# Kernel tuning notes

Measured on AMD Instinct MI355X. Metric: run time of the kernel, lower is better.

## Reference

```python
import jax, jax.numpy as jnp
import numpy as np

SEQ, BS, DIM = 2048, 2, 256
G, NQ = 2, 8           # n_keys groups, n_queries total
SUB = NQ // G          # queries per group
EPS = 1e-5


def _ln(x, gamma, beta):
    m = jnp.mean(x, axis=-1, keepdims=True)
    v = jnp.mean(jnp.square(x - m), axis=-1, keepdims=True)
    return (x - m) * jax.lax.rsqrt(v + EPS) * gamma + beta


def setup_inputs() -> dict:
    key = jax.random.key(0)
    ks = jax.random.split(key, 16)
    s = 0.02
    return {
        "x":   jax.random.normal(ks[0], (SEQ, BS, DIM), jnp.float32),
        # block layernorms
        "g0": jnp.ones((DIM,), jnp.float32), "b0": jnp.zeros((DIM,), jnp.float32),
        "g1": jnp.ones((DIM,), jnp.float32), "b1": jnp.zeros((DIM,), jnp.float32),
        # attention q/k layernorm (norm_kvs=True)
        "gn": jnp.ones((DIM,), jnp.float32), "bn": jnp.zeros((DIM,), jnp.float32),
        # attention projections (torch Linear: weight [out,in])
        "wk": jax.random.normal(ks[1], (DIM * G, DIM), jnp.float32) * s,
        "bk": jnp.zeros((DIM * G,), jnp.float32),
        "wv": jax.random.normal(ks[2], (DIM * G, DIM), jnp.float32) * s,
        "bv": jnp.zeros((DIM * G,), jnp.float32),
        "wq": jax.random.normal(ks[3], (DIM * NQ, DIM), jnp.float32) * s,
        "bq": jnp.zeros((DIM * NQ,), jnp.float32),
        "wo": jax.random.normal(ks[4], (DIM, DIM * NQ), jnp.float32) * s,
        "bo": jnp.zeros((DIM,), jnp.float32),
        # FFN: BayesLora(dim,2dim) -> relu -> BayesLora(2dim,dim), eval == plain linear
        "w1": jax.random.normal(ks[5], (2 * DIM, DIM), jnp.float32) * s,
        "bf1": jnp.zeros((2 * DIM,), jnp.float32),
        "w2": jax.random.normal(ks[6], (DIM, 2 * DIM), jnp.float32) * s,
        "bf2": jnp.zeros((DIM,), jnp.float32),
    }


def reference(x, g0, b0, g1, b1, gn, bn, wk, bk, wv, bv, wq, bq, wo, bo, w1, bf1, w2, bf2):
    seq, bs, dim = x.shape
    # --- attention (pre-norm) ---
    h = _ln(x, g0, b0)                                        # s b d
    K = (h @ wk.T + bk).reshape(seq, bs, G, dim)              # s b g i
    V = (h @ wv.T + bv).reshape(seq, bs, G, dim)              # s b g i
    Q = (h @ wq.T + bq).reshape(seq, bs, G, SUB, dim)         # s b g u i
    K = _ln(K, gn, bn)
    Q = _ln(Q, gn, bn)
    scores = jnp.einsum('sbgui,tbgi->bgust', Q, K) / jnp.sqrt(jnp.float32(dim))
    neg = jnp.finfo(scores.dtype).min
    causal = jnp.tril(jnp.ones((seq, seq), bool))             # s1 >= s2 allowed
    scores = jnp.where(causal, scores, neg)
    probs = jax.nn.softmax(scores, axis=-1)                   # b g u s t
    out = jnp.einsum('bgust,tbgi->sbgui', probs, V)
    out = out.reshape(seq, bs, G * SUB * dim)                 # s b (g u i)
    x = x + (out @ wo.T + bo)
    # --- FFN (pre-norm) ---
    h2 = _ln(x, g1, b1)
    f = jax.nn.relu(h2 @ w1.T + bf1) @ w2.T + bf2
    return x + f
```

## Files before the change

kernel.cpp:

```cpp
#include <hip/hip_runtime.h>
#include <hip/hip_bf16.h>

#define SEQ  2048
#define BSZ  2
#define DIM  256
#define NG   2
#define NQH  8
#define SUBQ 4
#define ROWS (SEQ*BSZ)
#define NQKV 3072
#define QROW 6144

typedef unsigned int uint32;
typedef unsigned short ushort;
typedef __attribute__((ext_vector_type(8))) short short8;
typedef __attribute__((ext_vector_type(4))) float f32x4;

__device__ __forceinline__ float bflo(uint32 u){
  union { uint32 i; float f; } c; c.i = u << 16; return c.f;
}
__device__ __forceinline__ float bfhi(uint32 u){
  union { uint32 i; float f; } c; c.i = u & 0xffff0000u; return c.f;
}
__device__ __forceinline__ uint32 pack2(float a, float b){
  __hip_bfloat16 ha = __float2bfloat16(a);
  __hip_bfloat16 hb = __float2bfloat16(b);
  unsigned short ua, ub;
  __builtin_memcpy(&ua, &ha, 2);
  __builtin_memcpy(&ub, &hb, 2);
  return (uint32)ua | ((uint32)ub << 16);
}
__device__ __forceinline__ ushort bf16bits(float v){
  __hip_bfloat16 h = __float2bfloat16(v);
  ushort u; __builtin_memcpy(&u, &h, 2); return u;
}

__device__ __forceinline__ void dma16(const void* g, void* l) {
  __builtin_amdgcn_global_load_lds(
      (const __attribute__((address_space(1))) uint32*)g,
      (__attribute__((address_space(3))) uint32*)l, 16, 0, 0);
}

__device__ __forceinline__ size_t op2_addr(size_t o2) {
  return (o2 >> 11) * QROW + (o2 & 1023) + ((o2 >> 10) & 1) * 3072;
}

__global__ __launch_bounds__(256) void misc0(
    const float* __restrict__ wk, const float* __restrict__ wv,
    const float* __restrict__ wq, const float* __restrict__ wo,
    const float* __restrict__ w1, const float* __restrict__ w2,
    const float* __restrict__ bk, const float* __restrict__ bv,
    const float* __restrict__ bq,
    __hip_bfloat16* __restrict__ out, float* __restrict__ bc,
    const float* __restrict__ x, const float* __restrict__ g0,
    const float* __restrict__ b0, __hip_bfloat16* __restrict__ Hf)
{
  if (blockIdx.x < 771) {
    int u = blockIdx.x * 256 + threadIdx.x;
    if (u < 196608) {
      int lane = u & 63, col = lane & 15, quad = lane >> 4;
      const float* srcrow;
      if (u < 98304) {
        int n16 = u >> 9, kc = (u >> 6) & 7;
        int n = n16 * 16 + col;
        const float* m = (n < 512) ? (wk + (size_t)n * 256)
                       : (n < 1024) ? (wv + (size_t)(n - 512) * 256)
                                    : (wq + (size_t)(n - 1024) * 256);
        srcrow = m + kc * 32 + quad * 8;
      } else if (u < 163840) {
        int local = u - 98304;
        int n16 = local >> 12, kc = (local >> 6) & 63;
        srcrow = wo + (size_t)(n16 * 16 + col) * 2048 + kc * 32 + quad * 8;
      } else if (u < 180224) {
        int local = u - 163840;
        int n16 = local >> 9, kc = (local >> 6) & 7;
        srcrow = w1 + (size_t)(n16 * 16 + col) * 256 + kc * 32 + quad * 8;
      } else {
        int local = u - 180224;
        int n16 = local >> 10, kc = (local >> 6) & 15;
        srcrow = w2 + (size_t)(n16 * 16 + col) * 512 + kc * 32 + quad * 8;
      }
      float4 a = *(const float4*)srcrow;
      float4 b = *(const float4*)(srcrow + 4);
      uint4 st;
      st.x = pack2(a.x, a.y); st.y = pack2(a.z, a.w);
      st.z = pack2(b.x, b.y); st.w = pack2(b.z, b.w);
      *(uint4*)((ushort*)out + (size_t)u * 8) = st;
    } else {
      int bu = u - 196608;
      const float* src; int loc;
      if      (bu < 128) { src = bk; loc = bu; }
      else if (bu < 256) { src = bv; loc = bu - 128; }
      else               { src = bq; loc = bu - 256; }
      *(float4*)(bc + 4 * (size_t)bu) = *(const float4*)(src + 4 * (size_t)loc);
    }
  } else {
    int wave = threadIdx.x >> 6, lane = threadIdx.x & 63;
    int row = (blockIdx.x - 771) * 4 + wave;
    size_t base = (size_t)row * DIM + lane * 4;
    float4 v = *(const float4*)(x + base);
    float s  = v.x + v.y + v.z + v.w;
    float s2 = v.x*v.x + v.y*v.y + v.z*v.z + v.w*v.w;
    #pragma unroll
    for (int o = 1; o < 64; o <<= 1) {
      s  += __shfl_xor(s, o);
      s2 += __shfl_xor(s2, o);
    }
    float m = s * (1.0f / DIM);
    float rb = rsqrtf(s2 * (1.0f / DIM) - m * m + 1e-5f);
    float4 gm = *(const float4*)(g0 + lane * 4);
    float4 bt = *(const float4*)(b0 + lane * 4);
    uint2 st;
    st.x = pack2((v.x - m) * rb * gm.x + bt.x, (v.y - m) * rb * gm.y + bt.y);
    st.y = pack2((v.z - m) * rb * gm.z + bt.z, (v.w - m) * rb * gm.w + bt.w);
    int kc = lane >> 3, quad = (lane >> 1) & 3, jj = 4 * (lane & 1);
    int cid = (row >> 4) * 8 + kc;
    *(uint2*)((ushort*)Hf + (size_t)cid * 512 + (quad * 16 + (row & 15)) * 8 + jj) = st;
  }
}

__global__ __launch_bounds__(256) void ln_swz(
    __hip_bfloat16* __restrict__ QKV,
    const float* __restrict__ gamma, const float* __restrict__ beta,
    __hip_bfloat16* __restrict__ Kf, __hip_bfloat16* __restrict__ Vf)
{
  int j = blockIdx.x;
  if (j < 10240) {
    int wave = threadIdx.x >> 6, lane = threadIdx.x & 63;
    int idx = j * 4 + wave;
    size_t base;
    if (idx < 8192) base = (size_t)(idx >> 1) * NQKV + (idx & 1) * DIM;
    else {
      int qi = idx - 8192;
      base = (size_t)(qi >> 3) * NQKV + 2 * NG * DIM + (qi & 7) * DIM;
    }
    __hip_bfloat16* p = QKV + base + lane * 4;
    uint2 u = *(const uint2*)p;
    float v0 = bflo(u.x), v1 = bfhi(u.x), v2 = bflo(u.y), v3 = bfhi(u.y);
    float s  = v0 + v1 + v2 + v3;
    float s2 = v0*v0 + v1*v1 + v2*v2 + v3*v3;
    #pragma unroll
    for (int o = 1; o < 64; o <<= 1) {
      s  += __shfl_xor(s, o);
      s2 += __shfl_xor(s2, o);
    }
    float m = s * (1.0f / DIM);
    float rb = rsqrtf(s2 * (1.0f / DIM) - m * m + 1e-5f);
    float4 gm = *(const float4*)(gamma + lane * 4);
    float4 bt = *(const float4*)(beta + lane * 4);
    uint2 st;
    st.x = pack2((v0 - m) * rb * gm.x + bt.x, (v1 - m) * rb * gm.y + bt.y);
    st.y = pack2((v2 - m) * rb * gm.z + bt.z, (v3 - m) * rb * gm.w + bt.w);
    if (idx < 8192) {
      int r = idx >> 1, gg = idx & 1;
      int t = r >> 1, b = r & 1;
      int bg = b * NG + gg;
      int kt = t >> 5, tr = t & 31, tc = tr >> 4, col = tr & 15;
      int ks = lane >> 3, quad = (lane >> 1) & 3, jj = 4 * (lane & 1);
      int cid = (bg * 64 + kt) * 16 + tc * 8 + ks;
      *(uint2*)((ushort*)Kf + (size_t)cid * 512 + (quad * 16 + col) * 8 + jj) = st;
    } else {
      *(uint2*)p = st;
    }
  } else {
    __shared__ ushort T[64][72];
    int vb = j - 10240;
    int t0 = (vb & 31) * 64, d0 = ((vb >> 5) & 3) * 64, bg = vb >> 7;
    int b = bg >> 1, g = bg & 1;
    int tid = threadIdx.x;
    int tr = tid >> 2, c4 = (tid & 3) * 16;
    const ushort* src = (const ushort*)QKV + ((size_t)(t0 + tr) * BSZ + b) * NQKV
                      + NG * DIM + g * DIM + d0 + c4;
    uint4 a0 = *(const uint4*)src;
    uint4 a1 = *(const uint4*)(src + 8);
    *(uint4*)&T[tr][c4]     = a0;
    *(uint4*)&T[tr][c4 + 8] = a1;
    __syncthreads();
    #pragma unroll
    for (int k2 = 0; k2 < 2; ++k2) {
      int u = tid * 2 + k2;
      int tt = u >> 8, di = (u >> 6) & 3, qd = (u >> 4) & 3, cl = u & 15;
      ushort tmp[8];
      #pragma unroll
      for (int e = 0; e < 8; ++e) tmp[e] = T[tt * 32 + qd * 8 + e][di * 16 + cl];
      int kt = (t0 >> 5) + tt;
      int dc = (d0 >> 4) + di;
      *(uint4*)((ushort*)Vf + (((size_t)(bg * 64 + kt) * 16 + dc) << 9) + (qd * 16 + cl) * 8)
          = *(uint4*)tmp;
    }
  }
}

template<int GN, int RELU, int OUTMODE, int AFRAG>
__global__ __launch_bounds__(256) void gemm_mfma(
    const __hip_bfloat16* __restrict__ A,
    const __hip_bfloat16* __restrict__ W,
    const float* __restrict__ bias,
    const float* __restrict__ resid,
    void* __restrict__ outp,
    int M, int N, int K)
{
  constexpr int WCH = GN / 16;
  constexpr int MC  = (GN == 128) ? 4 : 2;
  __shared__ __align__(16) ushort AS[2][4096];
  __shared__ __align__(16) ushort WS[2][WCH * 512];

  const int tid = threadIdx.x;
  const int wave = tid >> 6, lane = tid & 63;
  const int col = lane & 15, quad = lane >> 4;
  const int wm = (GN == 128) ? (wave >> 1) : wave;
  const int wn = (GN == 128) ? (wave & 1) : 0;
  const int bn0 = blockIdx.x * GN;
  const int bm0 = blockIdx.y * 128;
  const bool SPLIT = (OUTMODE == 2 || OUTMODE == 4);
  const int Keff  = SPLIT ? (K / gridDim.z) : K;
  const int kbase = SPLIT ? blockIdx.z * Keff : 0;
  const int kiters = Keff >> 5;

  f32x4 acc[MC][4];
  #pragma unroll
  for (int mc = 0; mc < MC; ++mc)
    #pragma unroll
    for (int nc = 0; nc < 4; ++nc)
      acc[mc][nc] = (f32x4){0.f, 0.f, 0.f, 0.f};

  auto stage = [&](int it, int bufi) {
    int k0 = kbase + it * 32;
    #pragma unroll
    for (int c = 0; c < 2; ++c) {
      int ch = wave * 2 + c;
      if (AFRAG)
        dma16((const ushort*)A + ((((size_t)(bm0 >> 4) + ch) * (K >> 5) + (k0 >> 5)) << 9) + lane * 8,
              &AS[bufi][ch * 512]);
      else
        dma16((const ushort*)A + (size_t)(bm0 + ch * 16 + col) * K + k0 + quad * 8,
              &AS[bufi][ch * 512]);
    }
    #pragma unroll
    for (int c = 0; c < WCH / 4; ++c) {
      int ch = wave * (WCH / 4) + c;
      dma16((const ushort*)W + (((size_t)((bn0 >> 4) + ch) * (K >> 5) + (k0 >> 5)) << 9) + lane * 8,
            &WS[bufi][ch * 512]);
    }
  };

  stage(0, 0);
  for (int it = 0; it < kiters; ++it) {
    int cur = it & 1;
    __syncthreads();
    if (it + 1 < kiters) stage(it + 1, 1 - cur);
    short8 af[MC], bf_[4];
    #pragma unroll
    for (int mc = 0; mc < MC; ++mc)
      af[mc] = *(const short8*)&AS[cur][(wm * MC + mc) * 512 + lane * 8];
    #pragma unroll
    for (int nc = 0; nc < 4; ++nc)
      bf_[nc] = *(const short8*)&WS[cur][(wn * 4 + nc) * 512 + lane * 8];
    #pragma unroll
    for (int mc = 0; mc < MC; ++mc)
      #pragma unroll
      for (int nc = 0; nc < 4; ++nc)
        acc[mc][nc] = __builtin_amdgcn_mfma_f32_16x16x32_bf16(af[mc], bf_[nc], acc[mc][nc], 0, 0, 0);
  }

  #pragma unroll
  for (int nc = 0; nc < 4; ++nc) {
    int n = bn0 + wn * 64 + nc * 16 + col;
    float bv = 0.f;
    if (OUTMODE == 0 || OUTMODE == 1 || OUTMODE == 3) bv = bias[n];
    #pragma unroll
    for (int mc = 0; mc < MC; ++mc) {
      #pragma unroll
      for (int reg = 0; reg < 4; ++reg) {
        int m = bm0 + wm * (MC * 16) + mc * 16 + quad * 4 + reg;
        float v = acc[mc][nc][reg] + bv;
        if ((OUTMODE == 0 || OUTMODE == 1 || OUTMODE == 3) && resid)
          v += resid[(size_t)m * N + n];
        if (RELU) v = fmaxf(v, 0.f);
        if (OUTMODE == 0)
          ((__hip_bfloat16*)outp)[(size_t)m * N + n] = __float2bfloat16(v);
        else if (OUTMODE == 1)
          ((float*)outp)[(size_t)m * N + n] = v;
        else if (OUTMODE == 2)
          ((float*)outp)[(size_t)blockIdx.z * M * N + (size_t)m * N + n] = v;
        else if (OUTMODE == 3) {
          int cid = (m >> 4) * (N >> 5) + (n >> 5);
          int kl = n & 31;
          ((ushort*)outp)[(size_t)cid * 512 + ((kl >> 3) * 16 + (m & 15)) * 8 + (kl & 7)] = bf16bits(v);
        } else {
          ((ushort*)outp)[(size_t)blockIdx.z * M * N + (size_t)m * N + n] = bf16bits(v);
        }
      }
    }
  }
}

__global__ __launch_bounds__(256) void combine2(
    const ushort* __restrict__ P, const float* __restrict__ bias,
    const float* __restrict__ resid, float* __restrict__ out, int MN)
{
  int i4 = (blockIdx.x * 256 + threadIdx.x) * 4;
  uint2 a = *(const uint2*)(P + i4);
  uint2 b = *(const uint2*)(P + MN + i4);
  float4 r = *(const float4*)(resid + i4);
  float4 bb = *(const float4*)(bias + (i4 & (DIM - 1)));
  float4 o;
  o.x = bflo(a.x) + bflo(b.x) + r.x + bb.x;
  o.y = bfhi(a.x) + bfhi(b.x) + r.y + bb.y;
  o.z = bflo(a.y) + bflo(b.y) + r.z + bb.z;
  o.w = bfhi(a.y) + bfhi(b.y) + r.w + bb.w;
  *(float4*)(out + i4) = o;
}

__global__ __launch_bounds__(256) void combine_ln4(
    const ushort* __restrict__ P, const float* __restrict__ bias,
    const float* __restrict__ resid, float* __restrict__ X2,
    const float* __restrict__ gamma, const float* __restrict__ beta,
    __hip_bfloat16* __restrict__ H2f)
{
  const int MN = ROWS * DIM;
  int wave = threadIdx.x >> 6, lane = threadIdx.x & 63;
  int row = blockIdx.x * 4 + wave;
  size_t i = (size_t)row * DIM + lane * 4;
  uint2 a = *(const uint2*)(P + i);
  uint2 b = *(const uint2*)(P + MN + i);
  uint2 c = *(const uint2*)(P + 2 * (size_t)MN + i);
  uint2 d = *(const uint2*)(P + 3 * (size_t)MN + i);
  float4 r = *(const float4*)(resid + i);
  float4 bb = *(const float4*)(bias + lane * 4);
  float4 v;
  v.x = bflo(a.x) + bflo(b.x) + bflo(c.x) + bflo(d.x) + r.x + bb.x;
  v.y = bfhi(a.x) + bfhi(b.x) + bfhi(c.x) + bfhi(d.x) + r.y + bb.y;
  v.z = bflo(a.y) + bflo(b.y) + bflo(c.y) + bflo(d.y) + r.z + bb.z;
  v.w = bfhi(a.y) + bfhi(b.y) + bfhi(c.y) + bfhi(d.y) + r.w + bb.w;
  *(float4*)(X2 + i) = v;
  float s  = v.x + v.y + v.z + v.w;
  float s2 = v.x*v.x + v.y*v.y + v.z*v.z + v.w*v.w;
  #pragma unroll
  for (int o = 1; o < 64; o <<= 1) {
    s  += __shfl_xor(s, o);
    s2 += __shfl_xor(s2, o);
  }
  float m = s * (1.0f / DIM);
  float rb = rsqrtf(s2 * (1.0f / DIM) - m * m + 1e-5f);
  float4 gm = *(const float4*)(gamma + lane * 4);
  float4 bt = *(const float4*)(beta + lane * 4);
  uint2 st;
  st.x = pack2((v.x - m) * rb * gm.x + bt.x, (v.y - m) * rb * gm.y + bt.y);
  st.y = pack2((v.z - m) * rb * gm.z + bt.z, (v.w - m) * rb * gm.w + bt.w);
  int kc = lane >> 3, quad = (lane >> 1) & 3, jj = 4 * (lane & 1);
  int cid = (row >> 4) * 8 + kc;
  *(uint2*)((ushort*)H2f + (size_t)cid * 512 + (quad * 16 + (row & 15)) * 8 + jj) = st;
}

__constant__ int C_NIT[32] = {22,22,22,21,21,20,20,20,20,20,20,19,19,18,18,18,18,17,17,16,16,16,16,16,16,14,14,12,12,12, 8, 4};
__constant__ int C_QB [32] = {10,10,15,15,15, 4, 9, 9,14,14,14,13,13,13, 8, 8,12,12,12, 3, 7, 7,11,11,11, 6, 6, 2, 5, 5, 1, 0};
__constant__ int C_Z  [32] = { 0, 1, 0, 1, 2, 0, 0, 1, 0, 1, 2, 0, 1, 2, 0, 1, 0, 1, 2, 0, 0, 1, 0, 1, 2, 0, 1, 0, 0, 1, 0, 0};
__constant__ int C_K0 [32] = { 0,22, 0,22,43, 0, 0,20, 0,20,40, 0,19,38, 0,18, 0,18,35, 0, 0,16, 0,16,32, 0,14, 0, 0,12, 0, 0};
__constant__ int C_SP [32] = { 1, 1, 1, 1, 1, 0, 1, 1, 1, 1, 1, 1, 1, 1, 1, 1, 1, 1, 1, 0, 1, 1, 1, 1, 1, 1, 1, 0, 1, 1, 0, 0};

__global__ __launch_bounds__(256, 2) void attn_mfma(
    const __hip_bfloat16* QKV,
    const __hip_bfloat16* __restrict__ Kf,
    const __hip_bfloat16* __restrict__ Vf,
    __hip_bfloat16* __restrict__ Obf,
    __hip_bfloat16* __restrict__ Op1f,
    ushort* Op2q,
    float* __restrict__ Lp)
{
  __shared__ __align__(16) ushort KS[2][8192];
  __shared__ __align__(16) ushort VS[2][8192];

  const int tid  = threadIdx.x;
  const int wave = tid >> 6, lane = tid & 63;
  const int col  = lane & 15, quad = lane >> 4;

  const int bid = blockIdx.x;
  const int x8 = bid & 7, j = bid >> 3;
  const int a = j >> 1, odd = j & 1;
  int rank;
  if (a < 16) rank = odd ? (31 - a) : a;
  else        rank = odd ? (a - 16) : (31 - (a - 16));
  const int head = odd * 8 + x8;
  const int qb  = C_QB[rank];
  const int z   = C_Z[rank];
  const int nit = C_NIT[rank];
  const int k0  = C_K0[rank];
  const int split = C_SP[rank];

  const int b = head >> 3, hq = head & 7, g = hq >> 2;
  const int bg = b * NG + g;
  const int qw0 = qb * 128 + wave * 32;

  short8 qf[2][8];
  #pragma unroll
  for (int mc = 0; mc < 2; ++mc) {
    int s = qw0 + mc * 16 + col;
    const ushort* qp = (const ushort*)QKV + (size_t)s * QROW + b * NQKV
                     + 2 * NG * DIM + hq * DIM + quad * 8;
    #pragma unroll
    for (int ks = 0; ks < 8; ++ks)
      qf[mc][ks] = *(const short8*)(qp + ks * 32);
  }

  short8 onesf;
  #pragma unroll
  for (int i = 0; i < 8; ++i) onesf[i] = (short)0x3F80;

  f32x4 o[2][16];
  #pragma unroll
  for (int mc = 0; mc < 2; ++mc)
    #pragma unroll
    for (int dc = 0; dc < 16; ++dc)
      o[mc][dc] = (f32x4){0.f, 0.f, 0.f, 0.f};
  float l_s[2][4] = {{0.f}};

  auto stage = [&](int i, int bufi) {
    int kt = k0 + i;
    const ushort* kb = (const ushort*)Kf + (((size_t)bg * 64 + kt) << 13);
    const ushort* vb = (const ushort*)Vf + (((size_t)bg * 64 + kt) << 13);
    #pragma unroll
    for (int cc = 0; cc < 4; ++cc) {
      int nk = wave * 4 + cc;
      dma16(kb + (nk << 9) + lane * 8, &KS[bufi][nk * 512]);
      dma16(vb + (nk << 9) + lane * 8, &VS[bufi][nk * 512]);
    }
  };

  const int sig0 = col + 16 * ((quad & 1) * 2);
  const int sig1 = sig0 + 16;

  stage(0, 0);
  for (int i = 0; i < nit; ++i) {
    int cur = i & 1;
    __syncthreads();
    if (i + 1 < nit) stage(i + 1, 1 - cur);
    int kt = k0 + i;
    if (kt * 32 > qw0 + 31) continue;

    f32x4 sf[2][2];
    #pragma unroll
    for (int mc = 0; mc < 2; ++mc)
      #pragma unroll
      for (int tc = 0; tc < 2; ++tc)
        sf[mc][tc] = (f32x4){0.f, 0.f, 0.f, 0.f};
    __builtin_amdgcn_s_setprio(1);
    #pragma unroll
    for (int ks = 0; ks < 8; ++ks) {
      short8 kb0 = *(const short8*)&KS[cur][ks * 512 + lane * 8];
      short8 kb1 = *(const short8*)&KS[cur][(8 + ks) * 512 + lane * 8];
      sf[0][0] = __builtin_amdgcn_mfma_f32_16x16x32_bf16(kb0, qf[0][ks], sf[0][0], 0, 0, 0);
      sf[0][1] = __builtin_amdgcn_mfma_f32_16x16x32_bf16(kb1, qf[0][ks], sf[0][1], 0, 0, 0);
      sf[1][0] = __builtin_amdgcn_mfma_f32_16x16x32_bf16(kb0, qf[1][ks], sf[1][0], 0, 0, 0);
      sf[1][1] = __builtin_amdgcn_mfma_f32_16x16x32_bf16(kb1, qf[1][ks], sf[1][1], 0, 0, 0);
    }
    __builtin_amdgcn_s_setprio(0);

    const bool dm = (kt * 32 + 31) > qw0;
    uint32 PK[2][2][2];
    #pragma unroll
    for (int mc = 0; mc < 2; ++mc)
      #pragma unroll
      for (int tc = 0; tc < 2; ++tc) {
        float p[4];
        #pragma unroll
        for (int reg = 0; reg < 4; ++reg) {
          p[reg] = __expf(sf[mc][tc][reg] * 0.0625f);
          if (dm) {
            int tg = kt * 32 + tc * 16 + quad * 4 + reg;
            int sg = qw0 + mc * 16 + col;
            if (tg > sg) p[reg] = 0.f;
          }
        }
        PK[mc][tc][0] = pack2(p[0], p[1]);
        PK[mc][tc][1] = pack2(p[2], p[3]);
      }

    short8 pa[2];
    #pragma unroll
    for (int mc = 0; mc < 2; ++mc) {
      union { uint32 u[4]; short8 s8; } cvt;
      #pragma unroll
      for (int dw = 0; dw < 4; ++dw) {
        int src = (dw < 2) ? sig0 : sig1;
        uint32 a0 = (uint32)__shfl((int)PK[mc][0][dw & 1], src, 64);
        uint32 a1 = (uint32)__shfl((int)PK[mc][1][dw & 1], src, 64);
        cvt.u[dw] = (quad < 2) ? a0 : a1;
      }
      pa[mc] = cvt.s8;
    }

    __builtin_amdgcn_s_setprio(1);
    f32x4 zz = (f32x4){0.f, 0.f, 0.f, 0.f};
    f32x4 ps0 = __builtin_amdgcn_mfma_f32_16x16x32_bf16(pa[0], onesf, zz, 0, 0, 0);
    f32x4 ps1 = __builtin_amdgcn_mfma_f32_16x16x32_bf16(pa[1], onesf, zz, 0, 0, 0);
    #pragma unroll
    for (int r = 0; r < 4; ++r) { l_s[0][r] += ps0[r]; l_s[1][r] += ps1[r]; }

    #pragma unroll
    for (int dc = 0; dc < 16; ++dc) {
      short8 vb = *(const short8*)&VS[cur][dc * 512 + lane * 8];
      o[0][dc] = __builtin_amdgcn_mfma_f32_16x16x32_bf16(pa[0], vb, o[0][dc], 0, 0, 0);
      o[1][dc] = __builtin_amdgcn_mfma_f32_16x16x32_bf16(pa[1], vb, o[1][dc], 0, 0, 0);
    }
    __builtin_amdgcn_s_setprio(0);
  }

  const int colh = col >> 3, coll = col & 7;
  #pragma unroll
  for (int mc = 0; mc < 2; ++mc)
    #pragma unroll
    for (int reg = 0; reg < 4; ++reg) {
      int s = qw0 + mc * 16 + quad * 4 + reg;
      int m = s * BSZ + b;
      int m16 = m >> 4, ml = m & 15;
      if (!split) {
        float inv = 1.0f / l_s[mc][reg];
        #pragma unroll
        for (int dc = 0; dc < 16; ++dc) {
          int cid = m16 * 64 + hq * 8 + (dc >> 1);
          int qt = (dc & 1) * 2 + colh;
          Obf[(size_t)cid * 512 + (qt * 16 + ml) * 8 + coll] =
              __float2bfloat16(o[mc][dc][reg] * inv);
        }
      } else {
        #pragma unroll
        for (int dc = 0; dc < 16; ++dc) {
          int qt = (dc & 1) * 2 + colh;
          int el = (qt * 16 + ml) * 8 + coll;
          float v = o[mc][dc][reg];
          if (z == 0) {
            Obf[((size_t)(m16 * 64 + hq * 8 + (dc >> 1))) * 512 + el] = __float2bfloat16(v);
          } else if (z == 1) {
            Op1f[((size_t)((m16 - 80) * 64 + hq * 8 + (dc >> 1))) * 512 + el] = __float2bfloat16(v);
          } else {
            size_t o2 = ((size_t)((m16 - 176) * 64 + hq * 8 + (dc >> 1))) * 512 + el;
            Op2q[op2_addr(o2)] = bf16bits(v);
          }
        }
        if (col == 0) Lp[((size_t)z * 2048 + s) * 16 + head] = l_s[mc][reg];
      }
    }
}

__global__ __launch_bounds__(256) void attn_norm(
    __hip_bfloat16* __restrict__ Obf, const __hip_bfloat16* __restrict__ Op1f,
    const ushort* __restrict__ Op2q, const float* __restrict__ Lp)
{
  int i8 = blockIdx.x * 256 + threadIdx.x;
  int cidr = i8 >> 6;
  int lane = i8 & 63;
  int m16r = cidr >> 6, kc = cidr & 63;
  int m16 = m16r + 80;
  int m = m16 * 16 + (lane & 15);
  int k = kc * 32 + (lane >> 4) * 8;
  int s = m >> 1, b = m & 1, hq = k >> 8;
  int head = b * 8 + hq;
  float l = Lp[(size_t)s * 16 + head] + Lp[(size_t)(2048 + s) * 16 + head];
  ushort* a = (ushort*)Obf + (((size_t)m16 * 64 + kc) << 9) + lane * 8;
  const ushort* c = (const ushort*)Op1f + (((size_t)m16r * 64 + kc) << 9) + lane * 8;
  uint4 ua = *(const uint4*)a;
  uint4 uc = *(const uint4*)c;
  float v0 = bflo(ua.x) + bflo(uc.x), v1 = bfhi(ua.x) + bfhi(uc.x);
  float v2 = bflo(ua.y) + bflo(uc.y), v3 = bfhi(ua.y) + bfhi(uc.y);
  float v4 = bflo(ua.z) + bflo(uc.z), v5 = bfhi(ua.z) + bfhi(uc.z);
  float v6 = bflo(ua.w) + bflo(uc.w), v7 = bfhi(ua.w) + bfhi(uc.w);
  if (s >= 1408) {
    l += Lp[(size_t)(4096 + s) * 16 + head];
    size_t o2 = (((size_t)(m16 - 176) * 64 + kc) << 9) + lane * 8;
    uint4 ue = *(const uint4*)(Op2q + op2_addr(o2));
    v0 += bflo(ue.x); v1 += bfhi(ue.x);
    v2 += bflo(ue.y); v3 += bfhi(ue.y);
    v4 += bflo(ue.z); v5 += bfhi(ue.z);
    v6 += bflo(ue.w); v7 += bfhi(ue.w);
  }
  float inv = 1.0f / l;
  uint4 st;
  st.x = pack2(v0 * inv, v1 * inv);
  st.y = pack2(v2 * inv, v3 * inv);
  st.z = pack2(v4 * inv, v5 * inv);
  st.w = pack2(v6 * inv, v7 * inv);
  *(uint4*)a = st;
}

extern "C" void kernel_launch(void* const* d_in, const int* in_sizes, int n_in,
                              void* d_out, int out_size, void* d_ws, size_t ws_size,
                              hipStream_t stream)
{
  const float* x   = (const float*)d_in[0];
  const float* g0  = (const float*)d_in[1];
  const float* b0  = (const float*)d_in[2];
  const float* g1  = (const float*)d_in[3];
  const float* b1  = (const float*)d_in[4];
  const float* gn  = (const float*)d_in[5];
  const float* bn  = (const float*)d_in[6];
  const float* wk  = (const float*)d_in[7];
  const float* bk  = (const float*)d_in[8];
  const float* wv  = (const float*)d_in[9];
  const float* bv  = (const float*)d_in[10];
  const float* wq  = (const float*)d_in[11];
  const float* bq  = (const float*)d_in[12];
  const float* wo  = (const float*)d_in[13];
  const float* bo  = (const float*)d_in[14];
  const float* w1  = (const float*)d_in[15];
  const float* bf1 = (const float*)d_in[16];
  const float* w2  = (const float*)d_in[17];
  const float* bf2 = (const float*)d_in[18];

  char* ws = (char*)d_ws;
  const size_t MB = 1024 * 1024;
  __hip_bfloat16* QKV = (__hip_bfloat16*)(ws);
  __hip_bfloat16* Pwo = (__hip_bfloat16*)(ws);
  __hip_bfloat16* Pw2 = (__hip_bfloat16*)(ws + 8  * MB);
  float*          X2  = (float*)         (ws + 16 * MB);
  __hip_bfloat16* H2f = (__hip_bfloat16*)(ws + 20 * MB);
  __hip_bfloat16* F1f = (__hip_bfloat16*)(ws + 22 * MB);
  __hip_bfloat16* Hf  = (__hip_bfloat16*)(ws + 24 * MB);
  __hip_bfloat16* Kf  = (__hip_bfloat16*)(ws + 24 * MB);
  __hip_bfloat16* Vf  = (__hip_bfloat16*)(ws + 28 * MB);
  __hip_bfloat16* Obf = (__hip_bfloat16*)(ws + 32 * MB);
  __hip_bfloat16* Op1f= (__hip_bfloat16*)(ws + 48 * MB);
  float*          BC  = (float*)         (ws + 59 * MB);
  float*          Lp  = (float*)         (ws + 59 * MB + 64 * 1024);
  __hip_bfloat16* WB  = (__hip_bfloat16*)(ws + 61 * MB);

  __hip_bfloat16* woB = WB + 786432;
  __hip_bfloat16* w1B = WB + 1310720;
  __hip_bfloat16* w2B = WB + 1441792;

  misc0<<<1795, 256, 0, stream>>>(wk, wv, wq, wo, w1, w2, bk, bv, bq, WB, BC, x, g0, b0, Hf);
  gemm_mfma<128,0,0,1><<<dim3(NQKV/128, ROWS/128), 256, 0, stream>>>(Hf, WB, BC, nullptr, QKV, ROWS, NQKV, DIM);
  ln_swz<<<12288, 256, 0, stream>>>(QKV, gn, bn, Kf, Vf);
  attn_mfma<<<512, 256, 0, stream>>>(QKV, Kf, Vf, Obf, Op1f, (ushort*)QKV, Lp);
  attn_norm<<<2816, 256, 0, stream>>>(Obf, Op1f, (const ushort*)QKV, Lp);
  gemm_mfma<64,0,4,1><<<dim3(DIM/64, ROWS/128, 4), 256, 0, stream>>>(Obf, woB, nullptr, nullptr, Pwo, ROWS, DIM, NQH*DIM);
  combine_ln4<<<ROWS / 4, 256, 0, stream>>>((const ushort*)Pwo, bo, x, X2, g1, b1, H2f);
  gemm_mfma<64,1,3,1><<<dim3((2*DIM)/64, ROWS/128), 256, 0, stream>>>(H2f, w1B, bf1, nullptr, F1f, ROWS, 2*DIM, DIM);
  gemm_mfma<64,0,4,1><<<dim3(DIM/64, ROWS/128, 2), 256, 0, stream>>>(F1f, w2B, nullptr, nullptr, Pw2, ROWS, DIM, 2*DIM);
  combine2<<<ROWS*DIM/1024, 256, 0, stream>>>((const ushort*)Pw2, bf2, X2, (float*)d_out, ROWS*DIM);
}
```

Baseline: 239.7 us.

## Split attention block into 8 waves of 16 query rows each

The attention kernel now runs 512 threads per block (8 waves) instead of 4, and each wave owns 16 query rows instead of 32. This halves per-wave accumulator and Q-fragment registers, so more waves can be resident per CU (launch bounds go from (256,2) to (512,4)). Each wave also issues half as many K/V DMA chunks per stage. The trade-off is that each K/V tile loaded into LDS is reused by fewer MFMAs per wave, and LDS reads and shuffles are repeated across twice as many waves.

```diff
diff --git a/kernel.cpp b/kernel.cpp
--- a/kernel.cpp
+++ b/kernel.cpp
@@ -359,7 +359,7 @@
 __constant__ int C_K0 [32] = { 0,22, 0,22,43, 0, 0,20, 0,20,40, 0,19,38, 0,18, 0,18,35, 0, 0,16, 0,16,32, 0,14, 0, 0,12, 0, 0};
 __constant__ int C_SP [32] = { 1, 1, 1, 1, 1, 0, 1, 1, 1, 1, 1, 1, 1, 1, 1, 1, 1, 1, 1, 0, 1, 1, 1, 1, 1, 1, 1, 0, 1, 1, 0, 0};
 
-__global__ __launch_bounds__(256, 2) void attn_mfma(
+__global__ __launch_bounds__(512, 4) void attn_mfma(
     const __hip_bfloat16* QKV,
     const __hip_bfloat16* __restrict__ Kf,
     const __hip_bfloat16* __restrict__ Vf,
@@ -390,38 +390,35 @@
 
   const int b = head >> 3, hq = head & 7, g = hq >> 2;
   const int bg = b * NG + g;
-  const int qw0 = qb * 128 + wave * 32;
-
-  short8 qf[2][8];
-  #pragma unroll
-  for (int mc = 0; mc < 2; ++mc) {
-    int s = qw0 + mc * 16 + col;
+  const int qw0 = qb * 128 + wave * 16;
+
+  short8 qf[8];
+  {
+    int s = qw0 + col;
     const ushort* qp = (const ushort*)QKV + (size_t)s * QROW + b * NQKV
                      + 2 * NG * DIM + hq * DIM + quad * 8;
     #pragma unroll
     for (int ks = 0; ks < 8; ++ks)
-      qf[mc][ks] = *(const short8*)(qp + ks * 32);
+      qf[ks] = *(const short8*)(qp + ks * 32);
   }
 
   short8 onesf;
   #pragma unroll
   for (int i = 0; i < 8; ++i) onesf[i] = (short)0x3F80;
 
-  f32x4 o[2][16];
+  f32x4 o[16];
   #pragma unroll
-  for (int mc = 0; mc < 2; ++mc)
-    #pragma unroll
-    for (int dc = 0; dc < 16; ++dc)
-      o[mc][dc] = (f32x4){0.f, 0.f, 0.f, 0.f};
-  float l_s[2][4] = {{0.f}};
+  for (int dc = 0; dc < 16; ++dc)
+    o[dc] = (f32x4){0.f, 0.f, 0.f, 0.f};
+  float l_s[4] = {0.f, 0.f, 0.f, 0.f};
 
   auto stage = [&](int i, int bufi) {
     int kt = k0 + i;
     const ushort* kb = (const ushort*)Kf + (((size_t)bg * 64 + kt) << 13);
     const ushort* vb = (const ushort*)Vf + (((size_t)bg * 64 + kt) << 13);
     #pragma unroll
-    for (int cc = 0; cc < 4; ++cc) {
-      int nk = wave * 4 + cc;
+    for (int cc = 0; cc < 2; ++cc) {
+      int nk = wave * 2 + cc;
       dma16(kb + (nk << 9) + lane * 8, &KS[bufi][nk * 512]);
       dma16(vb + (nk << 9) + lane * 8, &VS[bufi][nk * 512]);
     }
@@ -436,111 +433,99 @@
     __syncthreads();
     if (i + 1 < nit) stage(i + 1, 1 - cur);
     int kt = k0 + i;
-    if (kt * 32 > qw0 + 31) continue;
-
-    f32x4 sf[2][2];
-    #pragma unroll
-    for (int mc = 0; mc < 2; ++mc)
-      #pragma unroll
-      for (int tc = 0; tc < 2; ++tc)
-        sf[mc][tc] = (f32x4){0.f, 0.f, 0.f, 0.f};
+    if (kt * 32 > qw0 + 15) continue;
+
+    f32x4 sf[2];
+    sf[0] = (f32x4){0.f, 0.f, 0.f, 0.f};
+    sf[1] = (f32x4){0.f, 0.f, 0.f, 0.f};
     __builtin_amdgcn_s_setprio(1);
     #pragma unroll
     for (int ks = 0; ks < 8; ++ks) {
       short8 kb0 = *(const short8*)&KS[cur][ks * 512 + lane * 8];
       short8 kb1 = *(const short8*)&KS[cur][(8 + ks) * 512 + lane * 8];
-      sf[0][0] = __builtin_amdgcn_mfma_f32_16x16x32_bf16(kb0, qf[0][ks], sf[0][0], 0, 0, 0);
-      sf[0][1] = __builtin_amdgcn_mfma_f32_16x16x32_bf16(kb1, qf[0][ks], sf[0][1], 0, 0, 0);
-      sf[1][0] = __builtin_amdgcn_mfma_f32_16x16x32_bf16(kb0, qf[1][ks], sf[1][0], 0, 0, 0);
-      sf[1][1] = __builtin_amdgcn_mfma_f32_16x16x32_bf16(kb1, qf[1][ks], sf[1][1], 0, 0, 0);
+      sf[0] = __builtin_amdgcn_mfma_f32_16x16x32_bf16(kb0, qf[ks], sf[0], 0, 0, 0);
+      sf[1] = __builtin_amdgcn_mfma_f32_16x16x32_bf16(kb1, qf[ks], sf[1], 0, 0, 0);
     }
     __builtin_amdgcn_s_setprio(0);
 
     const bool dm = (kt * 32 + 31) > qw0;
-    uint32 PK[2][2][2];
-    #pragma unroll
-    for (int mc = 0; mc < 2; ++mc)
+    uint32 PK[2][2];
+    #pragma unroll
+    for (int tc = 0; tc < 2; ++tc) {
+      float p[4];
       #pragma unroll
-      for (int tc = 0; tc < 2; ++tc) {
-        float p[4];
-        #pragma unroll
-        for (int reg = 0; reg < 4; ++reg) {
-          p[reg] = __expf(sf[mc][tc][reg] * 0.0625f);
-          if (dm) {
-            int tg = kt * 32 + tc * 16 + quad * 4 + reg;
-            int sg = qw0 + mc * 16 + col;
-            if (tg > sg) p[reg] = 0.f;
-          }
+      for (int reg = 0; reg < 4; ++reg) {
+        p[reg] = __expf(sf[tc][reg] * 0.0625f);
+        if (dm) {
+          int tg = kt * 32 + tc * 16 + quad * 4 + reg;
+          int sg = qw0 + col;
+          if (tg > sg) p[reg] = 0.f;
         }
-        PK[mc][tc][0] = pack2(p[0], p[1]);
-        PK[mc][tc][1] = pack2(p[2], p[3]);
       }
-
-    short8 pa[2];
-    #pragma unroll
-    for (int mc = 0; mc < 2; ++mc) {
+      PK[tc][0] = pack2(p[0], p[1]);
+      PK[tc][1] = pack2(p[2], p[3]);
+    }
+
+    short8 pa;
+    {
       union { uint32 u[4]; short8 s8; } cvt;
       #pragma unroll
       for (int dw = 0; dw < 4; ++dw) {
         int src = (dw < 2) ? sig0 : sig1;
-        uint32 a0 = (uint32)__shfl((int)PK[mc][0][dw & 1], src, 64);
-        uint32 a1 = (uint32)__shfl((int)PK[mc][1][dw & 1], src, 64);
+        uint32 a0 = (uint32)__shfl((int)PK[0][dw & 1], src, 64);
+        uint32 a1 = (uint32)__shfl((int)PK[1][dw & 1], src, 64);
         cvt.u[dw] = (quad < 2) ? a0 : a1;
       }
-      pa[mc] = cvt.s8;
+      pa = cvt.s8;
     }
 
     __builtin_amdgcn_s_setprio(1);
     f32x4 zz = (f32x4){0.f, 0.f, 0.f, 0.f};
-    f32x4 ps0 = __builtin_amdgcn_mfma_f32_16x16x32_bf16(pa[0], onesf, zz, 0, 0, 0);
-    f32x4 ps1 = __builtin_amdgcn_mfma_f32_16x16x32_bf16(pa[1], onesf, zz, 0, 0, 0);
-    #pragma unroll
-    for (int r = 0; r < 4; ++r) { l_s[0][r] += ps0[r]; l_s[1][r] += ps1[r]; }
+    f32x4 ps = __builtin_amdgcn_mfma_f32_16x16x32_bf16(pa, onesf, zz, 0, 0, 0);
+    #pragma unroll
+    for (int r = 0; r < 4; ++r) l_s[r] += ps[r];
 
     #pragma unroll
     for (int dc = 0; dc < 16; ++dc) {
       short8 vb = *(const short8*)&VS[cur][dc * 512 + lane * 8];
-      o[0][dc] = __builtin_amdgcn_mfma_f32_16x16x32_bf16(pa[0], vb, o[0][dc], 0, 0, 0);
-      o[1][dc] = __builtin_amdgcn_mfma_f32_16x16x32_bf16(pa[1], vb, o[1][dc], 0, 0, 0);
+      o[dc] = __builtin_amdgcn_mfma_f32_16x16x32_bf16(pa, vb, o[dc], 0, 0, 0);
     }
     __builtin_amdgcn_s_setprio(0);
   }
 
   const int colh = col >> 3, coll = col & 7;
   #pragma unroll
-  for (int mc = 0; mc < 2; ++mc)
-    #pragma unroll
-    for (int reg = 0; reg < 4; ++reg) {
-      int s = qw0 + mc * 16 + quad * 4 + reg;
-      int m = s * BSZ + b;
-      int m16 = m >> 4, ml = m & 15;
-      if (!split) {
-        float inv = 1.0f / l_s[mc][reg];
-        #pragma unroll
-        for (int dc = 0; dc < 16; ++dc) {
-          int cid = m16 * 64 + hq * 8 + (dc >> 1);
-          int qt = (dc & 1) * 2 + colh;
-          Obf[(size_t)cid * 512 + (qt * 16 + ml) * 8 + coll] =
-              __float2bfloat16(o[mc][dc][reg] * inv);
+  for (int reg = 0; reg < 4; ++reg) {
+    int s = qw0 + quad * 4 + reg;
+    int m = s * BSZ + b;
+    int m16 = m >> 4, ml = m & 15;
+    if (!split) {
+      float inv = 1.0f / l_s[reg];
+      #pragma unroll
+      for (int dc = 0; dc < 16; ++dc) {
+        int cid = m16 * 64 + hq * 8 + (dc >> 1);
+        int qt = (dc & 1) * 2 + colh;
+        Obf[(size_t)cid * 512 + (qt * 16 + ml) * 8 + coll] =
+            __float2bfloat16(o[dc][reg] * inv);
+      }
+    } else {
+      #pragma unroll
+      for (int dc = 0; dc < 16; ++dc) {
+        int qt = (dc & 1) * 2 + colh;
+        int el = (qt * 16 + ml) * 8 + coll;
+        float v = o[dc][reg];
+        if (z == 0) {
+          Obf[((size_t)(m16 * 64 + hq * 8 + (dc >> 1))) * 512 + el] = __float2bfloat16(v);
+        } else if (z == 1) {
+          Op1f[((size_t)((m16 - 80) * 64 + hq * 8 + (dc >> 1))) * 512 + el] = __float2bfloat16(v);
+        } else {
+          size_t o2 = ((size_t)((m16 - 176) * 64 + hq * 8 + (dc >> 1))) * 512 + el;
+          Op2q[op2_addr(o2)] = bf16bits(v);
         }
-      } else {
-        #pragma unroll
-        for (int dc = 0; dc < 16; ++dc) {
-          int qt = (dc & 1) * 2 + colh;
-          int el = (qt * 16 + ml) * 8 + coll;
-          float v = o[mc][dc][reg];
-          if (z == 0) {
-            Obf[((size_t)(m16 * 64 + hq * 8 + (dc >> 1))) * 512 + el] = __float2bfloat16(v);
-          } else if (z == 1) {
-            Op1f[((size_t)((m16 - 80) * 64 + hq * 8 + (dc >> 1))) * 512 + el] = __float2bfloat16(v);
-          } else {
-            size_t o2 = ((size_t)((m16 - 176) * 64 + hq * 8 + (dc >> 1))) * 512 + el;
-            Op2q[op2_addr(o2)] = bf16bits(v);
-          }
-        }
-        if (col == 0) Lp[((size_t)z * 2048 + s) * 16 + head] = l_s[mc][reg];
       }
-    }
+      if (col == 0) Lp[((size_t)z * 2048 + s) * 16 + head] = l_s[reg];
+    }
+  }
 }
 
 __global__ __launch_bounds__(256) void attn_norm(
@@ -631,7 +616,7 @@
   misc0<<<1795, 256, 0, stream>>>(wk, wv, wq, wo, w1, w2, bk, bv, bq, WB, BC, x, g0, b0, Hf);
   gemm_mfma<128,0,0,1><<<dim3(NQKV/128, ROWS/128), 256, 0, stream>>>(Hf, WB, BC, nullptr, QKV, ROWS, NQKV, DIM);
   ln_swz<<<12288, 256, 0, stream>>>(QKV, gn, bn, Kf, Vf);
-  attn_mfma<<<512, 256, 0, stream>>>(QKV, Kf, Vf, Obf, Op1f, (ushort*)QKV, Lp);
+  attn_mfma<<<512, 512, 0, stream>>>(QKV, Kf, Vf, Obf, Op1f, (ushort*)QKV, Lp);
   attn_norm<<<2816, 256, 0, stream>>>(Obf, Op1f, (const ushort*)QKV, Lp);
   gemm_mfma<64,0,4,1><<<dim3(DIM/64, ROWS/128, 4), 256, 0, stream>>>(Obf, woB, nullptr, nullptr, Pwo, ROWS, DIM, NQH*DIM);
   combine_ln4<<<ROWS / 4, 256, 0, stream>>>((const ushort*)Pwo, bo, x, X2, g1, b1, H2f);
```

Result: no change. 236.0 us (median of 3 runs) (-1.5%).
